# Kernel optimization log

Hardware: AMD Instinct MI355X
Metric: run time of the kernel (lower is better)

The kernel has to match this reference:

```python
import jax, jax.numpy as jnp
import numpy as np

N_NODES = 50000
N_EDGES = 1600000
N_PAIRS = 4096
IN_N, IN_E = 32, 8
H, OE, ON = 4, 8, 32  # heads, out_edge_feats, out_node_feats
L = 4  # layers


def setup_inputs() -> dict:
    key = jax.random.key(0)
    ks = jax.random.split(key, 20)
    s = 0.1
    return {
        "x": jax.random.normal(ks[0], (N_NODES, IN_N), jnp.float32),
        "e": jax.random.normal(ks[1], (N_EDGES, IN_E), jnp.float32),
        "W_ni": jax.random.normal(ks[2], (L, IN_N, H * OE), jnp.float32) * s,
        "W_nj": jax.random.normal(ks[3], (L, IN_N, H * OE), jnp.float32) * s,
        "W_fij": jax.random.normal(ks[4], (L, IN_E, H * OE), jnp.float32) * s,
        "b_edge": jax.random.normal(ks[5], (L, H * OE), jnp.float32) * s,
        "attn": jax.random.normal(ks[6], (L, H, OE), jnp.float32) * s,
        "W_node": jax.random.normal(ks[7], (L, IN_N, H * ON), jnp.float32) * s,
        "W1": jax.random.normal(ks[8], (2 * L * ON, 128), jnp.float32) * s,
        "b1": jax.random.normal(ks[9], (128,), jnp.float32) * s,
        "W2": jax.random.normal(ks[10], (128, 1), jnp.float32) * s,
        "b2": jax.random.normal(ks[11], (1,), jnp.float32) * s,
        "src": jax.random.randint(ks[12], (N_EDGES,), 0, N_NODES, jnp.int32),
        "dst": jax.random.randint(ks[13], (N_EDGES,), 0, N_NODES, jnp.int32),
        "users": jax.random.randint(ks[14], (N_PAIRS,), 0, N_NODES, jnp.int32),
        "items": jax.random.randint(ks[15], (N_PAIRS,), 0, N_NODES, jnp.int32),
    }


def _egat_layer(h, e, src, dst, W_ni, W_nj, W_fij, b_edge, attn, W_node, n_nodes):
    # per-edge edge features: f_ni[src] + f_nj[dst] + f_fij + bias  -> (E, H*OE)
    f = (h @ W_ni)[src] + (h @ W_nj)[dst] + e @ W_fij + b_edge
    f_out = jax.nn.leaky_relu(f).reshape(-1, H, OE)          # (E, H, OE)
    logits = jnp.einsum("ehd,hd->eh", f_out, attn)           # (E, H)
    # edge softmax over incoming edges of each dst node
    mx = jax.ops.segment_max(logits, dst, num_segments=n_nodes)
    z = jnp.exp(logits - mx[dst])
    denom = jax.ops.segment_sum(z, dst, num_segments=n_nodes)
    a = z / denom[dst]                                        # (E, H)
    hh = (h @ W_node).reshape(n_nodes, H, ON)                 # (N, H, ON)
    msg = hh[src] * a[:, :, None]                             # (E, H, ON)
    return jax.ops.segment_sum(msg, dst, num_segments=n_nodes)  # (N, H, ON)


def reference(x, e, W_ni, W_nj, W_fij, b_edge, attn, W_node, W1, b1, W2, b2,
              src, dst, users, items):
    n_nodes = x.shape[0]
    states = []
    h = x
    for l in range(L):
        agg = _egat_layer(h, e, src, dst, W_ni[l], W_nj[l], W_fij[l],
                          b_edge[l], attn[l], W_node[l], n_nodes)
        h = jax.nn.elu(agg.sum(axis=1))  # sum heads, ELU -> (N, ON)
        states.append(h)
    states = jnp.concatenate(states, axis=1)                  # (N, L*ON)
    z = jnp.concatenate([states[users], states[items]], axis=1)  # (B, 2*L*ON)
    z = jax.nn.relu(z @ W1 + b1)
    out = jax.nn.sigmoid(z @ W2 + b2)
    return out[:, 0]
```

## Files before the change

kernel.cpp:

```cpp
#include <hip/hip_runtime.h>
#include <math.h>


static __device__ inline unsigned short f2bf(float f) {
  unsigned x = __float_as_uint(f);
  unsigned r = x + 0x7fffu + ((x >> 16) & 1u);
  return (unsigned short)(r >> 16);
}
static __device__ inline unsigned pack2bf(float lo, float hi) {
  return (unsigned)f2bf(lo) | ((unsigned)f2bf(hi) << 16);
}
static __device__ inline float bf2f(unsigned short u) {
  return __uint_as_float(((unsigned)u) << 16);
}
static __device__ inline float bf_lo(unsigned u) {
  return __uint_as_float(u << 16);
}
static __device__ inline float bf_hi(unsigned u) {
  return __uint_as_float(u & 0xffff0000u);
}


__global__ void zero_ints(int* __restrict__ p, int n) {
  int i = blockIdx.x * blockDim.x + threadIdx.x;
  if (i < n) p[i] = 0;
}

__global__ void histogram(const int* __restrict__ dst, int* __restrict__ hist,
                          int n_edges) {
  int e = blockIdx.x * blockDim.x + threadIdx.x;
  if (e < n_edges) atomicAdd(&hist[dst[e]], 1);
}

__global__ void scan_block(const int* __restrict__ hist, int* __restrict__ partial,
                           int* __restrict__ blocksum, int n) {
  __shared__ int buf[1024];
  int tid = threadIdx.x;
  int g = blockIdx.x * 1024 + tid;
  int v = (g < n) ? hist[g] : 0;
  buf[tid] = v;
  __syncthreads();
  for (int off = 1; off < 1024; off <<= 1) {
    int t = (tid >= off) ? buf[tid - off] : 0;
    __syncthreads();
    buf[tid] += t;
    __syncthreads();
  }
  if (g < n) partial[g] = buf[tid] - v;
  if (tid == 1023) blocksum[blockIdx.x] = buf[1023];
}

__global__ void scan_sums(int* __restrict__ blocksum, int nb) {
  if (threadIdx.x == 0 && blockIdx.x == 0) {
    int run = 0;
    for (int i = 0; i < nb; i++) {
      int t = blocksum[i];
      blocksum[i] = run;
      run += t;
    }
    blocksum[nb] = run;
  }
}

__global__ void scan_add(int* __restrict__ partial ,
                         const int* __restrict__ blocksum,
                         int* __restrict__ cursor, int n, int nb) {
  int g = blockIdx.x * blockDim.x + threadIdx.x;
  if (g < n) {
    int val = partial[g] + blocksum[g >> 10];
    partial[g] = val;
    cursor[g] = val;
  }
  if (g == 0) partial[n] = blocksum[nb];
}

#define FILL_NR 8
__global__ void fill_perm3(const int* __restrict__ dst, const int* __restrict__ src,
                           int* __restrict__ cursor, int* __restrict__ perm,
                           int* __restrict__ src_s, int* __restrict__ dst_s,
                           int n_edges, int seg) {
  int range = blockIdx.x % FILL_NR;
  int group = blockIdx.x / FILL_NR;
  int ngroups = gridDim.x / FILL_NR;
  int lo = range * seg;
  int hi = lo + seg;
  int stride = ngroups * blockDim.x;
  for (int k = group * blockDim.x + threadIdx.x; k < n_edges; k += stride) {
    int d = dst[k];
    if (d >= lo && d < hi) {
      int p = atomicAdd(&cursor[d], 1);
      perm[p] = k;
      src_s[p] = src[k];
      dst_s[p] = d;
    }
  }
}

__global__ void expand_e(const int* __restrict__ perm, const float* __restrict__ e,
                         uint4* __restrict__ e_s, int n_edges) {
  int k = blockIdx.x * blockDim.x + threadIdx.x;
  if (k >= n_edges) return;
  int eid = perm[k];
  const float4* ep = (const float4*)(e + (size_t)eid * 8);
  float4 a = ep[0], b = ep[1];
  uint4 r;
  r.x = pack2bf(a.x, a.y); r.y = pack2bf(a.z, a.w);
  r.z = pack2bf(b.x, b.y); r.w = pack2bf(b.z, b.w);
  e_s[k] = r;
}


__global__ void node_proj(const float* __restrict__ h,
                          const float* __restrict__ Wni,
                          const float* __restrict__ Wnj,
                          const float* __restrict__ Wnode,
                          const float* __restrict__ bE,
                          unsigned short* __restrict__ fni,
                          unsigned short* __restrict__ cdst,
                          unsigned short* __restrict__ hh_t, int n_nodes) {
  int wave = (blockIdx.x * blockDim.x + threadIdx.x) >> 6;
  int lane = threadIdx.x & 63;
  int nwaves = (gridDim.x * blockDim.x) >> 6;
  int j = lane & 31;
  size_t plane = (size_t)n_nodes * 32;
  const float* Wsel = (lane < 32) ? Wni : Wnj;
  for (int n = wave; n < n_nodes; n += nwaves) {
    const float* hrow = h + (size_t)n * 32;
    float a0 = 0.f, a1 = 0.f, a2 = 0.f;
#pragma unroll
    for (int k = 0; k < 32; k++) {
      float hv = hrow[k];
      a0 += hv * Wsel[k * 32 + j];
      a1 += hv * Wnode[k * 128 + lane];
      a2 += hv * Wnode[k * 128 + lane + 64];
    }
    if (lane < 32) fni[(size_t)n * 32 + j] = f2bf(a0);
    else           cdst[(size_t)n * 32 + j] = f2bf(a0 + bE[j]);
    int h0 = lane >> 5;
    int h1 = 2 + (lane >> 5);
    hh_t[h0 * plane + (size_t)n * 32 + j] = f2bf(a1);
    hh_t[h1 * plane + (size_t)n * 32 + j] = f2bf(a2);
  }
}

__global__ void edge_z(const int* __restrict__ src_s,
                       const int* __restrict__ dst_s,
                       const uint4* __restrict__ e_s,
                       const unsigned short* __restrict__ fni,
                       const unsigned short* __restrict__ cdst,
                       const float* __restrict__ Wf,
                       const float* __restrict__ attn,
                       float* __restrict__ zh, int n_edges) {
  __shared__ float wfl[256];
  __shared__ float atl[32];
  int tid = threadIdx.x;
  wfl[tid] = Wf[tid];
  if (tid < 32) atl[tid] = attn[tid];
  __syncthreads();
  int k = blockIdx.x * blockDim.x + tid;
  if (k >= n_edges) return;
  int s = src_s[k], d = dst_s[k];
  uint4 ep = e_s[k];
  float ev[8];
  ev[0] = bf_lo(ep.x); ev[1] = bf_hi(ep.x);
  ev[2] = bf_lo(ep.y); ev[3] = bf_hi(ep.y);
  ev[4] = bf_lo(ep.z); ev[5] = bf_hi(ep.z);
  ev[6] = bf_lo(ep.w); ev[7] = bf_hi(ep.w);
  const uint4* fr = (const uint4*)(fni + (size_t)s * 32);
  const uint4* cr = (const uint4*)(cdst + (size_t)d * 32);
  float f[32];
#pragma unroll
  for (int q = 0; q < 4; q++) {
    uint4 ua = fr[q], ub = cr[q];
    const unsigned* uap = (const unsigned*)&ua;
    const unsigned* ubp = (const unsigned*)&ub;
#pragma unroll
    for (int c = 0; c < 4; c++) {
      int jj = q * 8 + c * 2;
      f[jj]     = bf_lo(uap[c]) + bf_lo(ubp[c]);
      f[jj + 1] = bf_hi(uap[c]) + bf_hi(ubp[c]);
    }
  }
#pragma unroll
  for (int kk = 0; kk < 8; kk++) {
    float ek = ev[kk];
#pragma unroll
    for (int j4 = 0; j4 < 8; j4++) {
      float4 w = ((const float4*)wfl)[kk * 8 + j4];
      f[j4 * 4 + 0] = fmaf(ek, w.x, f[j4 * 4 + 0]);
      f[j4 * 4 + 1] = fmaf(ek, w.y, f[j4 * 4 + 1]);
      f[j4 * 4 + 2] = fmaf(ek, w.z, f[j4 * 4 + 2]);
      f[j4 * 4 + 3] = fmaf(ek, w.w, f[j4 * 4 + 3]);
    }
  }
  float lg[4] = {0.f, 0.f, 0.f, 0.f};
#pragma unroll
  for (int jj = 0; jj < 32; jj++) {
    float t = f[jj];
    t = (t >= 0.f) ? t : 0.01f * t;
    lg[jj >> 3] = fmaf(t, atl[jj], lg[jj >> 3]);
  }
  zh[k]                       = __expf(lg[0]);
  zh[(size_t)n_edges + k]     = __expf(lg[1]);
  zh[2 * (size_t)n_edges + k] = __expf(lg[2]);
  zh[3 * (size_t)n_edges + k] = __expf(lg[3]);
}

__global__ void node_agg_head(const float* __restrict__ zh,
                              const int* __restrict__ src_s,
                              const int* __restrict__ row_off,
                              const unsigned* __restrict__ hh_t,
                              unsigned* __restrict__ outh,
                              int n_nodes, int n_edges) {
  __shared__ float zb[4][64];
  __shared__ int sb[4][64];
  int wid = threadIdx.x >> 6;
  int lane = threadIdx.x & 63;
  int xcd = blockIdx.x & 7;
  int head = xcd >> 1;
  int i = (blockIdx.x >> 3) * 2 + (xcd & 1);
  int n = i * 4 + wid;
  if (n >= n_nodes) return;
  const float* z = zh + (size_t)head * n_edges;
  const unsigned* hs = hh_t + (size_t)head * n_nodes * 16;
  float* zw = zb[wid];
  int* sw = sb[wid];
  int g = lane >> 4, fl = lane & 15;
  int base = row_off[n], end = row_off[n + 1];
  float accx = 0.f, accy = 0.f, sz = 0.f;

  for (int chunk = base; chunk < end; chunk += 64) {
    int k = chunk + lane;
    float zv = 0.f;
    int sv = 0;
    if (k < end) { zv = z[k]; sv = src_s[k]; }
    zw[lane] = zv;
    sw[lane] = sv;
    sz += zv;
    int cnt = min(64, end - chunk);
    int iters = (cnt + 3) >> 2;
    int ee = 0;
    for (; ee + 4 <= iters; ee += 4) {
      unsigned u[4];
      float zl[4];
#pragma unroll
      for (int t = 0; t < 4; t++) {
        int idx = (ee + t) * 4 + g;
        zl[t] = zw[idx];
        int ss = sw[idx];
        u[t] = hs[(size_t)ss * 16 + fl];
      }
#pragma unroll
      for (int t = 0; t < 4; t++) {
        accx = fmaf(bf_lo(u[t]), zl[t], accx);
        accy = fmaf(bf_hi(u[t]), zl[t], accy);
      }
    }
    for (; ee < iters; ee++) {
      int idx = ee * 4 + g;
      float zl = zw[idx];
      int ss = sw[idx];
      unsigned u = hs[(size_t)ss * 16 + fl];
      accx = fmaf(bf_lo(u), zl, accx);
      accy = fmaf(bf_hi(u), zl, accy);
    }
  }

#pragma unroll
  for (int off = 32; off > 0; off >>= 1) sz += __shfl_xor(sz, off);
  accx += __shfl_xor(accx, 16); accx += __shfl_xor(accx, 32);
  accy += __shfl_xor(accy, 16); accy += __shfl_xor(accy, 32);
  if (lane < 16) {
    float ax = 0.f, ay = 0.f;
    if (sz > 0.f) { ax = accx / sz; ay = accy / sz; }
    outh[((size_t)head * n_nodes + n) * 16 + fl] = pack2bf(ax, ay);
  }
}

__global__ void combine(const unsigned* __restrict__ outh,
                        float* __restrict__ hcur,
                        unsigned* __restrict__ states_u,
                        int l, int n_nodes) {
  int idx = blockIdx.x * blockDim.x + threadIdx.x;
  if (idx >= n_nodes * 16) return;
  int n = idx >> 4, fl = idx & 15;
  size_t plane = (size_t)n_nodes * 16;
  unsigned a0 = outh[(size_t)n * 16 + fl];
  unsigned a1 = outh[plane + (size_t)n * 16 + fl];
  unsigned a2 = outh[2 * plane + (size_t)n * 16 + fl];
  unsigned a3 = outh[3 * plane + (size_t)n * 16 + fl];
  float vx = bf_lo(a0) + bf_lo(a1) + bf_lo(a2) + bf_lo(a3);
  float vy = bf_hi(a0) + bf_hi(a1) + bf_hi(a2) + bf_hi(a3);
  float rx = (vx > 0.f) ? vx : expm1f(vx);
  float ry = (vy > 0.f) ? vy : expm1f(vy);
  ((float2*)(hcur + (size_t)n * 32))[fl] = make_float2(rx, ry);
  states_u[(size_t)n * 64 + l * 16 + fl] = pack2bf(rx, ry);
}

__global__ void mlp_head(const unsigned short* __restrict__ states,
                         const int* __restrict__ users, const int* __restrict__ items,
                         const float* __restrict__ W1, const float* __restrict__ b1,
                         const float* __restrict__ W2, const float* __restrict__ b2,
                         float* __restrict__ out, int n_pairs) {
  __shared__ float zin[256];
  __shared__ float red[2];
  int p = blockIdx.x;
  if (p >= n_pairs) return;
  int t = threadIdx.x;
  int u = users[p], it = items[p];
  zin[t] = bf2f(states[(size_t)u * 128 + t]);
  zin[t + 128] = bf2f(states[(size_t)it * 128 + t]);
  __syncthreads();
  float acc = b1[t];
#pragma unroll 8
  for (int i = 0; i < 256; i++) acc += zin[i] * W1[i * 128 + t];
  acc = acc > 0.f ? acc : 0.f;
  float c = acc * W2[t];
#pragma unroll
  for (int off = 32; off > 0; off >>= 1) c += __shfl_down(c, off);
  if ((t & 63) == 0) red[t >> 6] = c;
  __syncthreads();
  if (t == 0) {
    float sum = red[0] + red[1] + b2[0];
    out[p] = 1.f / (1.f + expf(-sum));
  }
}


extern "C" void kernel_launch(void* const* d_in, const int* in_sizes, int n_in,
                              void* d_out, int out_size, void* d_ws, size_t ws_size,
                              hipStream_t stream) {
  const float* x     = (const float*)d_in[0];
  const float* e     = (const float*)d_in[1];
  const float* W_ni  = (const float*)d_in[2];
  const float* W_nj  = (const float*)d_in[3];
  const float* W_fij = (const float*)d_in[4];
  const float* b_e   = (const float*)d_in[5];
  const float* attn  = (const float*)d_in[6];
  const float* W_nd  = (const float*)d_in[7];
  const float* W1    = (const float*)d_in[8];
  const float* b1    = (const float*)d_in[9];
  const float* W2    = (const float*)d_in[10];
  const float* b2    = (const float*)d_in[11];
  const int* src   = (const int*)d_in[12];
  const int* dst   = (const int*)d_in[13];
  const int* users = (const int*)d_in[14];
  const int* items = (const int*)d_in[15];
  float* out = (float*)d_out;

  int n_nodes = in_sizes[0] / 32;
  int n_edges = in_sizes[12];
  int n_pairs = in_sizes[14];

  char* wsb = (char*)d_ws;
  size_t off = 0;
  auto alloc = [&](size_t bytes) {
    char* p = wsb + off;
    off = (off + bytes + 255) & ~(size_t)255;
    return p;
  };
  float*          hcur   = (float*)alloc((size_t)n_nodes * 32 * 4);
  unsigned*       states = (unsigned*)alloc((size_t)n_nodes * 64 * 4);
  unsigned short* fni    = (unsigned short*)alloc((size_t)n_nodes * 32 * 2);
  unsigned short* cdst   = (unsigned short*)alloc((size_t)n_nodes * 32 * 2);
  unsigned short* hh_t   = (unsigned short*)alloc((size_t)n_nodes * 128 * 2);
  uint4*          e_s    = (uint4*)alloc((size_t)n_edges * 16);
  float*          zh     = (float*)alloc((size_t)n_edges * 4 * 4);
  unsigned*       outh   = (unsigned*)alloc((size_t)n_nodes * 64 * 4);
  int*            src_s  = (int*)alloc((size_t)n_edges * 4);
  int*            dst_s  = (int*)alloc((size_t)n_edges * 4);
  int*            row_off  = (int*)alloc(((size_t)n_nodes + 8) * 4);
  int*            blocksum = (int*)alloc(256 * 4);
  int* perm   = (int*)outh;
  int* hist   = (int*)((char*)outh + ((size_t)n_edges * 4 + 1024));
  int* cursor = (int*)((char*)outh + ((size_t)n_edges * 4 + (size_t)(n_nodes + 16) * 4 + 2048));

  int nb = (n_nodes + 1023) / 1024;
  int seg = (n_nodes + FILL_NR - 1) / FILL_NR;
  zero_ints<<<(n_nodes + 255) / 256, 256, 0, stream>>>(hist, n_nodes);
  histogram<<<(n_edges + 255) / 256, 256, 0, stream>>>(dst, hist, n_edges);
  scan_block<<<nb, 1024, 0, stream>>>(hist, row_off, blocksum, n_nodes);
  scan_sums<<<1, 64, 0, stream>>>(blocksum, nb);
  scan_add<<<(n_nodes + 255) / 256, 256, 0, stream>>>(row_off, blocksum, cursor,
                                                      n_nodes, nb);
  fill_perm3<<<2048, 256, 0, stream>>>(dst, src, cursor, perm, src_s, dst_s,
                                       n_edges, seg);
  expand_e<<<(n_edges + 255) / 256, 256, 0, stream>>>(perm, e, e_s, n_edges);

  int aggblocks = 8 * ((((n_nodes + 3) / 4) + 1) / 2);
  for (int l = 0; l < 4; l++) {
    const float* hin = (l == 0) ? x : hcur;
    node_proj<<<2048, 256, 0, stream>>>(hin, W_ni + l * 1024, W_nj + l * 1024,
                                        W_nd + l * 4096, b_e + l * 32,
                                        fni, cdst, hh_t, n_nodes);
    edge_z<<<(n_edges + 255) / 256, 256, 0, stream>>>(
        src_s, dst_s, e_s, fni, cdst, W_fij + l * 256, attn + l * 32,
        zh, n_edges);
    node_agg_head<<<aggblocks, 256, 0, stream>>>(
        zh, src_s, row_off, (const unsigned*)hh_t, outh, n_nodes, n_edges);
    combine<<<(n_nodes * 16 + 255) / 256, 256, 0, stream>>>(
        outh, hcur, states, l, n_nodes);
  }
  mlp_head<<<n_pairs, 128, 0, stream>>>((const unsigned short*)states, users,
                                        items, W1, b1, W2, b2, out, n_pairs);
}
```

Baseline: 985.8 us.

## Pack edge records, store attention as fp16 per-edge, nontemporal loads/stores

Merges the src index and permutation into a single int2 record and fills dst_s by expanding the CSR row offsets instead of scattering it. Attention weights are stored as four fp16 values in one 8-byte record per edge, replacing four fp32 head planes, so edge_z writes and the aggregation reads less. The aggregation loop unroll goes from 4 to 8, nontemporal hints are added to many loads and stores, and the per-head outputs and states are widened from bf16 to fp32. The mix trades some bandwidth savings for larger fp32 intermediates, and fp16 may lose range on exp values compared with fp32.

```diff
diff --git a/kernel.cpp b/kernel.cpp
--- a/kernel.cpp
+++ b/kernel.cpp
@@ -1,6 +1,11 @@
 #include <hip/hip_runtime.h>
+#include <hip/hip_fp16.h>
 #include <math.h>
 
+
+typedef unsigned uv2 __attribute__((ext_vector_type(2)));
+typedef unsigned uv4 __attribute__((ext_vector_type(4)));
+typedef float fv2 __attribute__((ext_vector_type(2)));
 
 static __device__ inline unsigned short f2bf(float f) {
   unsigned x = __float_as_uint(f);
@@ -10,14 +15,21 @@
 static __device__ inline unsigned pack2bf(float lo, float hi) {
   return (unsigned)f2bf(lo) | ((unsigned)f2bf(hi) << 16);
 }
-static __device__ inline float bf2f(unsigned short u) {
-  return __uint_as_float(((unsigned)u) << 16);
-}
 static __device__ inline float bf_lo(unsigned u) {
   return __uint_as_float(u << 16);
 }
 static __device__ inline float bf_hi(unsigned u) {
   return __uint_as_float(u & 0xffff0000u);
+}
+static __device__ inline unsigned pack2h(float a, float b) {
+  __half2 h2 = __floats2half2_rn(a, b);
+  return *(unsigned*)&h2;
+}
+static __device__ inline float h_lo(unsigned u) {
+  return __half2float(__ushort_as_half((unsigned short)(u & 0xffffu)));
+}
+static __device__ inline float h_hi(unsigned u) {
+  return __half2float(__ushort_as_half((unsigned short)(u >> 16)));
 }
 
 
@@ -75,10 +87,9 @@
 }
 
 #define FILL_NR 8
-__global__ void fill_perm3(const int* __restrict__ dst, const int* __restrict__ src,
-                           int* __restrict__ cursor, int* __restrict__ perm,
-                           int* __restrict__ src_s, int* __restrict__ dst_s,
-                           int n_edges, int seg) {
+__global__ void fill_rec(const int* __restrict__ dst, const int* __restrict__ src,
+                         int* __restrict__ cursor, int2* __restrict__ rec,
+                         int n_edges, int seg) {
   int range = blockIdx.x % FILL_NR;
   int group = blockIdx.x / FILL_NR;
   int ngroups = gridDim.x / FILL_NR;
@@ -89,18 +100,24 @@
     int d = dst[k];
     if (d >= lo && d < hi) {
       int p = atomicAdd(&cursor[d], 1);
-      perm[p] = k;
-      src_s[p] = src[k];
-      dst_s[p] = d;
-    }
-  }
-}
-
-__global__ void expand_e(const int* __restrict__ perm, const float* __restrict__ e,
+      rec[p] = make_int2(src[k], k);
+    }
+  }
+}
+
+__global__ void dst_fill(const int* __restrict__ row_off, int* __restrict__ dst_s,
+                         int n_nodes) {
+  int n = blockIdx.x * blockDim.x + threadIdx.x;
+  if (n >= n_nodes) return;
+  int b = row_off[n], e = row_off[n + 1];
+  for (int k = b; k < e; k++) dst_s[k] = n;
+}
+
+__global__ void expand_e(const int2* __restrict__ rec, const float* __restrict__ e,
                          uint4* __restrict__ e_s, int n_edges) {
   int k = blockIdx.x * blockDim.x + threadIdx.x;
   if (k >= n_edges) return;
-  int eid = perm[k];
+  int eid = rec[k].y;
   const float4* ep = (const float4*)(e + (size_t)eid * 8);
   float4 a = ep[0], b = ep[1];
   uint4 r;
@@ -138,19 +155,19 @@
     else           cdst[(size_t)n * 32 + j] = f2bf(a0 + bE[j]);
     int h0 = lane >> 5;
     int h1 = 2 + (lane >> 5);
-    hh_t[h0 * plane + (size_t)n * 32 + j] = f2bf(a1);
-    hh_t[h1 * plane + (size_t)n * 32 + j] = f2bf(a2);
-  }
-}
-
-__global__ void edge_z(const int* __restrict__ src_s,
+    __builtin_nontemporal_store(f2bf(a1), &hh_t[h0 * plane + (size_t)n * 32 + j]);
+    __builtin_nontemporal_store(f2bf(a2), &hh_t[h1 * plane + (size_t)n * 32 + j]);
+  }
+}
+
+__global__ void edge_z(const int2* __restrict__ rec,
                        const int* __restrict__ dst_s,
                        const uint4* __restrict__ e_s,
                        const unsigned short* __restrict__ fni,
                        const unsigned short* __restrict__ cdst,
                        const float* __restrict__ Wf,
                        const float* __restrict__ attn,
-                       float* __restrict__ zh, int n_edges) {
+                       uv2* __restrict__ zrec, int n_edges) {
   __shared__ float wfl[256];
   __shared__ float atl[32];
   int tid = threadIdx.x;
@@ -159,8 +176,10 @@
   __syncthreads();
   int k = blockIdx.x * blockDim.x + tid;
   if (k >= n_edges) return;
-  int s = src_s[k], d = dst_s[k];
-  uint4 ep = e_s[k];
+  uv2 rc = __builtin_nontemporal_load((const uv2*)rec + k);
+  int s = (int)rc.x;
+  int d = __builtin_nontemporal_load(dst_s + k);
+  uv4 ep = __builtin_nontemporal_load((const uv4*)e_s + k);
   float ev[8];
   ev[0] = bf_lo(ep.x); ev[1] = bf_hi(ep.x);
   ev[2] = bf_lo(ep.y); ev[3] = bf_hi(ep.y);
@@ -200,18 +219,18 @@
     t = (t >= 0.f) ? t : 0.01f * t;
     lg[jj >> 3] = fmaf(t, atl[jj], lg[jj >> 3]);
   }
-  zh[k]                       = __expf(lg[0]);
-  zh[(size_t)n_edges + k]     = __expf(lg[1]);
-  zh[2 * (size_t)n_edges + k] = __expf(lg[2]);
-  zh[3 * (size_t)n_edges + k] = __expf(lg[3]);
-}
-
-__global__ void node_agg_head(const float* __restrict__ zh,
-                              const int* __restrict__ src_s,
+  uv2 zout;
+  zout.x = pack2h(__expf(lg[0]), __expf(lg[1]));
+  zout.y = pack2h(__expf(lg[2]), __expf(lg[3]));
+  __builtin_nontemporal_store(zout, zrec + k);
+}
+
+__global__ void node_agg_head(const uv2* __restrict__ zrec,
+                              const int2* __restrict__ rec,
                               const int* __restrict__ row_off,
                               const unsigned* __restrict__ hh_t,
-                              unsigned* __restrict__ outh,
-                              int n_nodes, int n_edges) {
+                              fv2* __restrict__ outh,
+                              int n_nodes) {
   __shared__ float zb[4][64];
   __shared__ int sb[4][64];
   int wid = threadIdx.x >> 6;
@@ -221,7 +240,6 @@
   int i = (blockIdx.x >> 3) * 2 + (xcd & 1);
   int n = i * 4 + wid;
   if (n >= n_nodes) return;
-  const float* z = zh + (size_t)head * n_edges;
   const unsigned* hs = hh_t + (size_t)head * n_nodes * 16;
   float* zw = zb[wid];
   int* sw = sb[wid];
@@ -233,25 +251,31 @@
     int k = chunk + lane;
     float zv = 0.f;
     int sv = 0;
-    if (k < end) { zv = z[k]; sv = src_s[k]; }
+    if (k < end) {
+      uv2 zz = __builtin_nontemporal_load(zrec + k);
+      unsigned word = (head & 2) ? zz.y : zz.x;
+      zv = (head & 1) ? h_hi(word) : h_lo(word);
+      uv2 rc = __builtin_nontemporal_load((const uv2*)rec + k);
+      sv = (int)rc.x;
+    }
     zw[lane] = zv;
     sw[lane] = sv;
     sz += zv;
     int cnt = min(64, end - chunk);
     int iters = (cnt + 3) >> 2;
     int ee = 0;
-    for (; ee + 4 <= iters; ee += 4) {
-      unsigned u[4];
-      float zl[4];
-#pragma unroll
-      for (int t = 0; t < 4; t++) {
+    for (; ee + 8 <= iters; ee += 8) {
+      unsigned u[8];
+      float zl[8];
+#pragma unroll
+      for (int t = 0; t < 8; t++) {
         int idx = (ee + t) * 4 + g;
         zl[t] = zw[idx];
         int ss = sw[idx];
         u[t] = hs[(size_t)ss * 16 + fl];
       }
 #pragma unroll
-      for (int t = 0; t < 4; t++) {
+      for (int t = 0; t < 8; t++) {
         accx = fmaf(bf_lo(u[t]), zl[t], accx);
         accy = fmaf(bf_hi(u[t]), zl[t], accy);
       }
@@ -273,31 +297,33 @@
   if (lane < 16) {
     float ax = 0.f, ay = 0.f;
     if (sz > 0.f) { ax = accx / sz; ay = accy / sz; }
-    outh[((size_t)head * n_nodes + n) * 16 + fl] = pack2bf(ax, ay);
-  }
-}
-
-__global__ void combine(const unsigned* __restrict__ outh,
+    fv2 r;
+    r.x = ax; r.y = ay;
+    __builtin_nontemporal_store(r, &outh[((size_t)head * n_nodes + n) * 16 + fl]);
+  }
+}
+
+__global__ void combine(const fv2* __restrict__ outh,
                         float* __restrict__ hcur,
-                        unsigned* __restrict__ states_u,
+                        float* __restrict__ states,
                         int l, int n_nodes) {
   int idx = blockIdx.x * blockDim.x + threadIdx.x;
   if (idx >= n_nodes * 16) return;
   int n = idx >> 4, fl = idx & 15;
   size_t plane = (size_t)n_nodes * 16;
-  unsigned a0 = outh[(size_t)n * 16 + fl];
-  unsigned a1 = outh[plane + (size_t)n * 16 + fl];
-  unsigned a2 = outh[2 * plane + (size_t)n * 16 + fl];
-  unsigned a3 = outh[3 * plane + (size_t)n * 16 + fl];
-  float vx = bf_lo(a0) + bf_lo(a1) + bf_lo(a2) + bf_lo(a3);
-  float vy = bf_hi(a0) + bf_hi(a1) + bf_hi(a2) + bf_hi(a3);
+  fv2 a0 = __builtin_nontemporal_load(&outh[(size_t)n * 16 + fl]);
+  fv2 a1 = __builtin_nontemporal_load(&outh[plane + (size_t)n * 16 + fl]);
+  fv2 a2 = __builtin_nontemporal_load(&outh[2 * plane + (size_t)n * 16 + fl]);
+  fv2 a3 = __builtin_nontemporal_load(&outh[3 * plane + (size_t)n * 16 + fl]);
+  float vx = a0.x + a1.x + a2.x + a3.x;
+  float vy = a0.y + a1.y + a2.y + a3.y;
   float rx = (vx > 0.f) ? vx : expm1f(vx);
   float ry = (vy > 0.f) ? vy : expm1f(vy);
   ((float2*)(hcur + (size_t)n * 32))[fl] = make_float2(rx, ry);
-  states_u[(size_t)n * 64 + l * 16 + fl] = pack2bf(rx, ry);
-}
-
-__global__ void mlp_head(const unsigned short* __restrict__ states,
+  ((float2*)(states + (size_t)n * 128 + l * 32))[fl] = make_float2(rx, ry);
+}
+
+__global__ void mlp_head(const float* __restrict__ states,
                          const int* __restrict__ users, const int* __restrict__ items,
                          const float* __restrict__ W1, const float* __restrict__ b1,
                          const float* __restrict__ W2, const float* __restrict__ b2,
@@ -308,8 +334,8 @@
   if (p >= n_pairs) return;
   int t = threadIdx.x;
   int u = users[p], it = items[p];
-  zin[t] = bf2f(states[(size_t)u * 128 + t]);
-  zin[t + 128] = bf2f(states[(size_t)it * 128 + t]);
+  zin[t] = states[(size_t)u * 128 + t];
+  zin[t + 128] = states[(size_t)it * 128 + t];
   __syncthreads();
   float acc = b1[t];
 #pragma unroll 8
@@ -360,20 +386,19 @@
     return p;
   };
   float*          hcur   = (float*)alloc((size_t)n_nodes * 32 * 4);
-  unsigned*       states = (unsigned*)alloc((size_t)n_nodes * 64 * 4);
+  float*          states = (float*)alloc((size_t)n_nodes * 128 * 4);
   unsigned short* fni    = (unsigned short*)alloc((size_t)n_nodes * 32 * 2);
   unsigned short* cdst   = (unsigned short*)alloc((size_t)n_nodes * 32 * 2);
   unsigned short* hh_t   = (unsigned short*)alloc((size_t)n_nodes * 128 * 2);
   uint4*          e_s    = (uint4*)alloc((size_t)n_edges * 16);
-  float*          zh     = (float*)alloc((size_t)n_edges * 4 * 4);
-  unsigned*       outh   = (unsigned*)alloc((size_t)n_nodes * 64 * 4);
-  int*            src_s  = (int*)alloc((size_t)n_edges * 4);
+  uv2*            zrec   = (uv2*)alloc((size_t)n_edges * 8);
+  int2*           rec    = (int2*)alloc((size_t)n_edges * 8);
   int*            dst_s  = (int*)alloc((size_t)n_edges * 4);
+  fv2*            outh   = (fv2*)alloc((size_t)n_nodes * 64 * 8);
   int*            row_off  = (int*)alloc(((size_t)n_nodes + 8) * 4);
   int*            blocksum = (int*)alloc(256 * 4);
-  int* perm   = (int*)outh;
-  int* hist   = (int*)((char*)outh + ((size_t)n_edges * 4 + 1024));
-  int* cursor = (int*)((char*)outh + ((size_t)n_edges * 4 + (size_t)(n_nodes + 16) * 4 + 2048));
+  int* hist   = (int*)outh;
+  int* cursor = (int*)((char*)outh + (size_t)(n_nodes + 16) * 4);
 
   int nb = (n_nodes + 1023) / 1024;
   int seg = (n_nodes + FILL_NR - 1) / FILL_NR;
@@ -383,24 +408,25 @@
   scan_sums<<<1, 64, 0, stream>>>(blocksum, nb);
   scan_add<<<(n_nodes + 255) / 256, 256, 0, stream>>>(row_off, blocksum, cursor,
                                                       n_nodes, nb);
-  fill_perm3<<<2048, 256, 0, stream>>>(dst, src, cursor, perm, src_s, dst_s,
-                                       n_edges, seg);
-  expand_e<<<(n_edges + 255) / 256, 256, 0, stream>>>(perm, e, e_s, n_edges);
-
-  int aggblocks = 8 * ((((n_nodes + 3) / 4) + 1) / 2);
+  fill_rec<<<2048, 256, 0, stream>>>(dst, src, cursor, rec, n_edges, seg);
+  dst_fill<<<(n_nodes + 255) / 256, 256, 0, stream>>>(row_off, dst_s, n_nodes);
+  expand_e<<<(n_edges + 255) / 256, 256, 0, stream>>>(rec, e, e_s, n_edges);
+
+  int ngroups = (((n_nodes + 3) / 4) + 1) / 2;
+  int aggblocks = 8 * ngroups;
   for (int l = 0; l < 4; l++) {
     const float* hin = (l == 0) ? x : hcur;
     node_proj<<<2048, 256, 0, stream>>>(hin, W_ni + l * 1024, W_nj + l * 1024,
                                         W_nd + l * 4096, b_e + l * 32,
                                         fni, cdst, hh_t, n_nodes);
     edge_z<<<(n_edges + 255) / 256, 256, 0, stream>>>(
-        src_s, dst_s, e_s, fni, cdst, W_fij + l * 256, attn + l * 32,
-        zh, n_edges);
+        rec, dst_s, e_s, fni, cdst, W_fij + l * 256, attn + l * 32,
+        zrec, n_edges);
     node_agg_head<<<aggblocks, 256, 0, stream>>>(
-        zh, src_s, row_off, (const unsigned*)hh_t, outh, n_nodes, n_edges);
+        zrec, rec, row_off, (const unsigned*)hh_t, outh, n_nodes);
     combine<<<(n_nodes * 16 + 255) / 256, 256, 0, stream>>>(
         outh, hcur, states, l, n_nodes);
   }
-  mlp_head<<<n_pairs, 128, 0, stream>>>((const unsigned short*)states, users,
-                                        items, W1, b1, W2, b2, out, n_pairs);
-}
+  mlp_head<<<n_pairs, 128, 0, stream>>>(states, users, items, W1, b1, W2, b2,
+                                        out, n_pairs);
+}
```

New measurement: 1.100 ms. 11.6% more time.
